# Kernel optimization log

Measured on AMD Instinct MI355X. Metric: run time of the kernel, lower is better.

The kernel has to match this reference:

```python
import jax, jax.numpy as jnp
import numpy as np

T = 1024
V = 512
K_BINS = jnp.array([1, 2, 3, 4, 5, 6, 7, 8, 12, 16, 24, 32, 48, 64, 96, 128], dtype=jnp.int32)
SPLIT_T = T // 2                      # int(T * 0.5)
CW = max(4, T // 20)                  # crossfade width = 51
FADE_START = SPLIT_T - CW // 2        # 487
FADE_END = SPLIT_T + CW // 2          # 537


def _early_weight():
    t = jnp.arange(T, dtype=jnp.float32)
    fade = 1.0 - (t - FADE_START) / (FADE_END - FADE_START)
    ew = jnp.where(t < FADE_START, 1.0, jnp.where(t < FADE_END, fade, 0.0))
    return ew.reshape(1, T, 1)


def setup_inputs() -> dict:
    key = jax.random.key(0)
    k = jax.random.split(key, 5)
    B = 64
    return {
        "x": jax.random.normal(k[0], (B, T, V), dtype=jnp.float32),
        "g_early_real": jax.random.normal(k[1], (V, 16), dtype=jnp.float32) * 0.1,
        "g_early_imag": jax.random.normal(k[2], (V, 16), dtype=jnp.float32) * 0.1,
        "g_late_real": jax.random.normal(k[3], (V, 16), dtype=jnp.float32) * 0.1,
        "g_late_imag": jax.random.normal(k[4], (V, 16), dtype=jnp.float32) * 0.1,
    }


def reference(x, g_early_real, g_early_imag, g_late_real, g_late_imag):
    # x: [B, T, V] real. rfft along time.
    X = jnp.fft.rfft(x, n=T, axis=1)              # [B, F, V] complex, F = T//2+1
    xb = X[:, K_BINS, :]                          # [B, K, V]
    # complex gain (1 + gr + i*gi), broadcast [1, K, V]
    g_e = (g_early_real + 1j * g_early_imag).T[None, :, :]
    g_l = (g_late_real + 1j * g_late_imag).T[None, :, :]
    Y_e = X.at[:, K_BINS, :].set(xb * (1.0 + g_e))
    Y_l = X.at[:, K_BINS, :].set(xb * (1.0 + g_l))
    y_early = jnp.fft.irfft(Y_e, n=T, axis=1)     # [B, T, V]
    y_late = jnp.fft.irfft(Y_l, n=T, axis=1)
    ew = _early_weight()
    return ew * y_early + (1.0 - ew) * y_late
```

## Files before the change

### kernel.cpp

```cpp
#include <hip/hip_runtime.h>
#include <math.h>

#define T_LEN 1024
#define VV 512
#define BB 64
#define NB 16
#define ANG_STEP 0.006135923151542565f
#define FADE_S 487
#define FADE_E 537

typedef float v2f __attribute__((ext_vector_type(2)));

__device__ constexpr int KB[NB] = {1,2,3,4,5,6,7,8,12,16,24,32,48,64,96,128};
__device__ constexpr float SGN[NB] = {-1.f, 1.f, -1.f, 1.f, -1.f, 1.f, -1.f, 1.f,
                                       1.f, 1.f,  1.f, 1.f,  1.f, 1.f,  1.f, 1.f};

__global__ __launch_bounds__(512, 1) void k_fused(const float* __restrict__ x,
                                                  const float* __restrict__ ger,
                                                  const float* __restrict__ gei,
                                                  const float* __restrict__ glr,
                                                  const float* __restrict__ gli,
                                                  float* __restrict__ Hg,
                                                  float* __restrict__ out) {
    const int b    = blockIdx.x;
    const int vc   = blockIdx.y;
    const int tid  = threadIdx.x;
    const int wave = tid >> 6;
    const int lane = tid & 63;

    __shared__ __align__(16) float4 tab4[512][8];
    __shared__ __align__(16) float  scr[4 * 128 * 8];

    for (int i = tid; i < 512 * 8; i += 512) {
        int t = i >> 3, m = i & 7;
        int j0 = 2 * m, j1 = 2 * m + 1;
        int idx0 = (KB[j0] * t) & (T_LEN - 1);
        int idx1 = (KB[j1] * t) & (T_LEN - 1);
        float s0, c0, s1, c1;
        sincosf(ANG_STEP * (float)idx0, &s0, &c0);
        sincosf(ANG_STEP * (float)idx1, &s1, &c1);
        tab4[t][m] = make_float4(c0, s0, c1, s1);
    }
    __syncthreads();

    float ar0[NB], ai0[NB], ar1[NB], ai1[NB];
#pragma unroll
    for (int j = 0; j < NB; ++j) { ar0[j] = ai0[j] = ar1[j] = ai1[j] = 0.f; }

    const int trow = wave * 128;
    const int ttab = trow & 511;
    const float2* xrd = (const float2*)(x + ((size_t)b * T_LEN + trow) * VV + vc * 128) + lane;

#define DFT_T(TT, AV)                                               \
    do {                                                            \
        _Pragma("unroll")                                           \
        for (int m = 0; m < 8; ++m) {                               \
            float4 cs = tab4[ttab + (TT)][m];                       \
            ar0[2*m]   = fmaf((AV).x, cs.x, ar0[2*m]);              \
            ai0[2*m]   = fmaf(-(AV).x, cs.y, ai0[2*m]);             \
            ar1[2*m]   = fmaf((AV).y, cs.x, ar1[2*m]);              \
            ai1[2*m]   = fmaf(-(AV).y, cs.y, ai1[2*m]);             \
            ar0[2*m+1] = fmaf((AV).x, cs.z, ar0[2*m+1]);            \
            ai0[2*m+1] = fmaf(-(AV).x, cs.w, ai0[2*m+1]);           \
            ar1[2*m+1] = fmaf((AV).y, cs.z, ar1[2*m+1]);            \
            ai1[2*m+1] = fmaf(-(AV).y, cs.w, ai1[2*m+1]);           \
        }                                                           \
    } while (0)

    {
        float2 a0 = xrd[(size_t)0 * 256];
        float2 a1 = xrd[(size_t)1 * 256];
        float2 a2 = xrd[(size_t)2 * 256];
        float2 a3 = xrd[(size_t)3 * 256];
        float2 a4 = xrd[(size_t)4 * 256];
        float2 a5 = xrd[(size_t)5 * 256];
        float2 a6 = xrd[(size_t)6 * 256];
        float2 a7 = xrd[(size_t)7 * 256];
#pragma unroll 1
        for (int i = 0; i < 120; i += 8) {
            float2 b0 = xrd[(size_t)(i +  8) * 256];
            float2 b1 = xrd[(size_t)(i +  9) * 256];
            float2 b2 = xrd[(size_t)(i + 10) * 256];
            float2 b3 = xrd[(size_t)(i + 11) * 256];
            float2 b4 = xrd[(size_t)(i + 12) * 256];
            float2 b5 = xrd[(size_t)(i + 13) * 256];
            float2 b6 = xrd[(size_t)(i + 14) * 256];
            float2 b7 = xrd[(size_t)(i + 15) * 256];
            DFT_T(i + 0, a0); DFT_T(i + 1, a1); DFT_T(i + 2, a2); DFT_T(i + 3, a3);
            DFT_T(i + 4, a4); DFT_T(i + 5, a5); DFT_T(i + 6, a6); DFT_T(i + 7, a7);
            a0 = b0; a1 = b1; a2 = b2; a3 = b3;
            a4 = b4; a5 = b5; a6 = b6; a7 = b7;
        }
        DFT_T(120, a0); DFT_T(121, a1); DFT_T(122, a2); DFT_T(123, a3);
        DFT_T(124, a4); DFT_T(125, a5); DFT_T(126, a6); DFT_T(127, a7);
    }
#undef DFT_T

    if (wave >= 4) {
#pragma unroll
        for (int j = 0; j < NB; ++j) {
            ar0[j] *= SGN[j]; ai0[j] *= SGN[j];
            ar1[j] *= SGN[j]; ai1[j] *= SGN[j];
        }
    }
    __syncthreads();

    const int v0 = lane * 2;
    float Xre_lo[2], Xre_hi[2], Xim_lo[2], Xim_hi[2];

#define RED_ROUND(SRC0, SRC1, JOFF, DST)                                   \
    do {                                                                   \
        if (wave < 4) {                                                    \
            _Pragma("unroll")                                              \
            for (int jj = 0; jj < 8; ++jj) {                               \
                scr[((size_t)wave * 128 + v0)     * 8 + jj] = SRC0[(JOFF) + jj]; \
                scr[((size_t)wave * 128 + v0 + 1) * 8 + jj] = SRC1[(JOFF) + jj]; \
            }                                                              \
        }                                                                  \
        __syncthreads();                                                   \
        if (wave >= 4) {                                                   \
            const int w2 = wave - 4;                                       \
            _Pragma("unroll")                                              \
            for (int jj = 0; jj < 8; ++jj) {                               \
                scr[((size_t)w2 * 128 + v0)     * 8 + jj] += SRC0[(JOFF) + jj]; \
                scr[((size_t)w2 * 128 + v0 + 1) * 8 + jj] += SRC1[(JOFF) + jj]; \
            }                                                              \
        }                                                                  \
        __syncthreads();                                                   \
        _Pragma("unroll")                                                  \
        for (int q = 0; q < 2; ++q) {                                      \
            const int c  = tid * 2 + q;                                    \
            const int vq = c >> 3, jq = c & 7;                             \
            DST[q] = scr[((size_t)0 * 128 + vq) * 8 + jq]                  \
                   + scr[((size_t)1 * 128 + vq) * 8 + jq]                  \
                   + scr[((size_t)2 * 128 + vq) * 8 + jq]                  \
                   + scr[((size_t)3 * 128 + vq) * 8 + jq];                 \
        }                                                                  \
        __syncthreads();                                                   \
    } while (0)

    RED_ROUND(ar0, ar1, 0, Xre_lo);
    RED_ROUND(ar0, ar1, 8, Xre_hi);
    RED_ROUND(ai0, ai1, 0, Xim_lo);
    RED_ROUND(ai0, ai1, 8, Xim_hi);
#undef RED_ROUND

    const float scale = 2.0f / (float)T_LEN;
    {
        float* hg = Hg + (size_t)b * 64 * VV;
#pragma unroll
        for (int q = 0; q < 2; ++q) {
            const int c  = tid * 2 + q;
            const int vq = c >> 3;
            const int vg = vc * 128 + vq;
#pragma unroll
            for (int half = 0; half < 2; ++half) {
                const int jq = (c & 7) + half * 8;
                const float Xr = half ? Xre_hi[q] : Xre_lo[q];
                const float Xi = half ? Xim_hi[q] : Xim_lo[q];
                float er = ger[vg * NB + jq], ei = gei[vg * NB + jq];
                float lr = glr[vg * NB + jq], li = gli[vg * NB + jq];
                float here  = (Xr * er - Xi * ei) * scale;
                float heimN = -(Xr * ei + Xi * er) * scale;
                float hlre  = (Xr * lr - Xi * li) * scale;
                float hlimN = -(Xr * li + Xi * lr) * scale;
                hg[(size_t)jq * VV + vg]        = here;
                hg[(size_t)(16 + jq) * VV + vg] = heimN;
                hg[(size_t)(32 + jq) * VV + vg] = hlre;
                hg[(size_t)(48 + jq) * VV + vg] = hlimN;
            }
        }
    }
    __syncthreads();

    float hr0[NB], hi0[NB], hr1[NB], hi1[NB];
    {
        const int qb = (wave < 4) ? 0 : 32;
        const float* hgr = Hg + (size_t)b * 64 * VV + vc * 128;
#pragma unroll
        for (int j = 0; j < NB; ++j) {
            const float sg = (wave >= 4) ? SGN[j] : 1.0f;
            hr0[j] = hgr[(size_t)(qb + j) * VV + v0]          * sg;
            hr1[j] = hgr[(size_t)(qb + j) * VV + v0 + 1]      * sg;
            hi0[j] = hgr[(size_t)(qb + 16 + j) * VV + v0]     * sg;
            hi1[j] = hgr[(size_t)(qb + 16 + j) * VV + v0 + 1] * sg;
        }
    }

    v2f* ow = (v2f*)(out + ((size_t)b * T_LEN + trow) * VV + vc * 128) + lane;

#define APPLY_T(TT, AV)                                                       \
    do {                                                                      \
        float s0 = 0.f, s1 = 0.f;                                             \
        _Pragma("unroll")                                                     \
        for (int m = 0; m < 8; ++m) {                                         \
            float4 cs = tab4[ttab + (TT)][m];                                 \
            s0 = fmaf(hr0[2*m], cs.x, s0);   s0 = fmaf(hi0[2*m], cs.y, s0);   \
            s1 = fmaf(hr1[2*m], cs.x, s1);   s1 = fmaf(hi1[2*m], cs.y, s1);   \
            s0 = fmaf(hr0[2*m+1], cs.z, s0); s0 = fmaf(hi0[2*m+1], cs.w, s0); \
            s1 = fmaf(hr1[2*m+1], cs.z, s1); s1 = fmaf(hi1[2*m+1], cs.w, s1); \
        }                                                                     \
        v2f ov; ov.x = (AV).x + s0; ov.y = (AV).y + s1;                       \
        __builtin_nontemporal_store(ov, &ow[(size_t)(TT) * 256]);             \
    } while (0)

    {
        float2 a0 = xrd[(size_t)0 * 256];
        float2 a1 = xrd[(size_t)1 * 256];
        float2 a2 = xrd[(size_t)2 * 256];
        float2 a3 = xrd[(size_t)3 * 256];
        float2 a4 = xrd[(size_t)4 * 256];
        float2 a5 = xrd[(size_t)5 * 256];
        float2 a6 = xrd[(size_t)6 * 256];
        float2 a7 = xrd[(size_t)7 * 256];
#pragma unroll 1
        for (int i = 0; i < 120; i += 8) {
            float2 b0 = xrd[(size_t)(i +  8) * 256];
            float2 b1 = xrd[(size_t)(i +  9) * 256];
            float2 b2 = xrd[(size_t)(i + 10) * 256];
            float2 b3 = xrd[(size_t)(i + 11) * 256];
            float2 b4 = xrd[(size_t)(i + 12) * 256];
            float2 b5 = xrd[(size_t)(i + 13) * 256];
            float2 b6 = xrd[(size_t)(i + 14) * 256];
            float2 b7 = xrd[(size_t)(i + 15) * 256];
            APPLY_T(i + 0, a0); APPLY_T(i + 1, a1); APPLY_T(i + 2, a2); APPLY_T(i + 3, a3);
            APPLY_T(i + 4, a4); APPLY_T(i + 5, a5); APPLY_T(i + 6, a6); APPLY_T(i + 7, a7);
            a0 = b0; a1 = b1; a2 = b2; a3 = b3;
            a4 = b4; a5 = b5; a6 = b6; a7 = b7;
        }
        APPLY_T(120, a0); APPLY_T(121, a1); APPLY_T(122, a2); APPLY_T(123, a3);
        APPLY_T(124, a4); APPLY_T(125, a5); APPLY_T(126, a6); APPLY_T(127, a7);
    }
#undef APPLY_T
}

__global__ __launch_bounds__(512) void k_fixup(const float* __restrict__ x,
                                               const float* __restrict__ H,
                                               float* __restrict__ out) {
    const int b   = blockIdx.x;
    const int tz  = blockIdx.y;
    const int tid = threadIdx.x;
    const int ts  = tz ? 512 : FADE_S;
    const int te  = tz ? FADE_E : 512;
    const int nt  = te - ts;

    __shared__ float2 tab[32][NB];
    for (int i = tid; i < nt * NB; i += 512) {
        int t = i >> 4, j = i & 15;
        int idx = (KB[j] * (ts + t)) & (T_LEN - 1);
        float ss, cc; sincosf(ANG_STEP * (float)idx, &ss, &cc);
        tab[t][j] = make_float2(cc, ss);
    }

    float er[NB], ei[NB], lr[NB], li[NB];
    const float* hp = H + (size_t)b * 64 * VV + tid;
#pragma unroll
    for (int j = 0; j < NB; ++j) {
        er[j] = hp[(size_t)j        * VV];
        ei[j] = hp[(size_t)(16 + j) * VV];
        lr[j] = hp[(size_t)(32 + j) * VV];
        li[j] = hp[(size_t)(48 + j) * VV];
    }
    __syncthreads();

    const float* xrd = x + ((size_t)b * T_LEN + ts) * VV + tid;
    float*       ow  = out + ((size_t)b * T_LEN + ts) * VV + tid;

    for (int t = 0; t < nt; ++t) {
        float av = xrd[(size_t)t * VV];
        const int tg = ts + t;
        float se = 0.f, sl = 0.f;
#pragma unroll
        for (int j = 0; j < NB; ++j) {
            float2 cs = tab[t][j];
            se = fmaf(er[j], cs.x, se); se = fmaf(ei[j], cs.y, se);
            sl = fmaf(lr[j], cs.x, sl); sl = fmaf(li[j], cs.y, sl);
        }
        float w = 1.0f - (float)(tg - FADE_S) * (1.0f / 50.0f);
        ow[(size_t)t * VV] = av + fmaf(w, se - sl, sl);
    }
}

extern "C" void kernel_launch(void* const* d_in, const int* in_sizes, int n_in,
                              void* d_out, int out_size, void* d_ws, size_t ws_size,
                              hipStream_t stream) {
    (void)in_sizes; (void)n_in; (void)out_size; (void)ws_size;
    const float* x   = (const float*)d_in[0];
    const float* ger = (const float*)d_in[1];
    const float* gei = (const float*)d_in[2];
    const float* glr = (const float*)d_in[3];
    const float* gli = (const float*)d_in[4];
    float* out = (float*)d_out;

    float* Hg = (float*)d_ws;

    k_fused<<<dim3(BB, 4), 512, 0, stream>>>(x, ger, gei, glr, gli, Hg, out);
    k_fixup<<<dim3(BB, 2), 512, 0, stream>>>(x, Hg, out);
}
```

Measured before the change: 112.7 us.

## Replace LDS twiddle table with per-thread recurrence rotation of twiddles

Drops the 64KB shared-memory sincos table and its setup, and instead has each thread generate twiddles on the fly with a complex rotation recurrence seeded by sincosf at its row start. This removes the LDS reads from the DFT and apply loops, and the per-wave sign flips, and relaxes launch_bounds to allow more than one block per CU. In exchange it adds 4 FMA-class ops per bin per time step, which raises ALU work. Accumulated rotation error over 128 steps may also reduce accuracy. The prefetch depth is cut from 8 to 4 rows to save registers.

```diff
diff --git a/kernel.cpp b/kernel.cpp
--- a/kernel.cpp
+++ b/kernel.cpp
@@ -12,59 +12,56 @@
 typedef float v2f __attribute__((ext_vector_type(2)));
 
 __device__ constexpr int KB[NB] = {1,2,3,4,5,6,7,8,12,16,24,32,48,64,96,128};
-__device__ constexpr float SGN[NB] = {-1.f, 1.f, -1.f, 1.f, -1.f, 1.f, -1.f, 1.f,
-                                       1.f, 1.f,  1.f, 1.f,  1.f, 1.f,  1.f, 1.f};
-
-__global__ __launch_bounds__(512, 1) void k_fused(const float* __restrict__ x,
-                                                  const float* __restrict__ ger,
-                                                  const float* __restrict__ gei,
-                                                  const float* __restrict__ glr,
-                                                  const float* __restrict__ gli,
-                                                  float* __restrict__ Hg,
-                                                  float* __restrict__ out) {
+__device__ constexpr float CWT[NB] = {
+    0.9999811753f, 0.9999247018f, 0.9998305818f, 0.9996988187f,
+    0.9995294175f, 0.9993223846f, 0.9990777278f, 0.9987954562f,
+    0.9972904567f, 0.9951847267f, 0.9891765100f, 0.9807852804f,
+    0.9569403357f, 0.9238795325f, 0.8314696123f, 0.7071067812f};
+__device__ constexpr float SWT[NB] = {
+    0.0061358846f, 0.0122715383f, 0.0184067299f, 0.0245412285f,
+    0.0306748032f, 0.0368072229f, 0.0429382569f, 0.0490676743f,
+    0.0735645636f, 0.0980171403f, 0.1467304745f, 0.1950903220f,
+    0.2902846773f, 0.3826834324f, 0.5555702330f, 0.7071067812f};
+
+__global__ __launch_bounds__(512) void k_fused(const float* __restrict__ x,
+                                               const float* __restrict__ ger,
+                                               const float* __restrict__ gei,
+                                               const float* __restrict__ glr,
+                                               const float* __restrict__ gli,
+                                               float* __restrict__ Hg,
+                                               float* __restrict__ out) {
     const int b    = blockIdx.x;
     const int vc   = blockIdx.y;
     const int tid  = threadIdx.x;
     const int wave = tid >> 6;
     const int lane = tid & 63;
 
-    __shared__ __align__(16) float4 tab4[512][8];
-    __shared__ __align__(16) float  scr[4 * 128 * 8];
-
-    for (int i = tid; i < 512 * 8; i += 512) {
-        int t = i >> 3, m = i & 7;
-        int j0 = 2 * m, j1 = 2 * m + 1;
-        int idx0 = (KB[j0] * t) & (T_LEN - 1);
-        int idx1 = (KB[j1] * t) & (T_LEN - 1);
-        float s0, c0, s1, c1;
-        sincosf(ANG_STEP * (float)idx0, &s0, &c0);
-        sincosf(ANG_STEP * (float)idx1, &s1, &c1);
-        tab4[t][m] = make_float4(c0, s0, c1, s1);
-    }
-    __syncthreads();
-
-    float ar0[NB], ai0[NB], ar1[NB], ai1[NB];
-#pragma unroll
-    for (int j = 0; j < NB; ++j) { ar0[j] = ai0[j] = ar1[j] = ai1[j] = 0.f; }
+    __shared__ __align__(16) float scr[4 * 128 * 8];
 
     const int trow = wave * 128;
-    const int ttab = trow & 511;
+    const int v0   = lane * 2;
     const float2* xrd = (const float2*)(x + ((size_t)b * T_LEN + trow) * VV + vc * 128) + lane;
 
-#define DFT_T(TT, AV)                                               \
-    do {                                                            \
-        _Pragma("unroll")                                           \
-        for (int m = 0; m < 8; ++m) {                               \
-            float4 cs = tab4[ttab + (TT)][m];                       \
-            ar0[2*m]   = fmaf((AV).x, cs.x, ar0[2*m]);              \
-            ai0[2*m]   = fmaf(-(AV).x, cs.y, ai0[2*m]);             \
-            ar1[2*m]   = fmaf((AV).y, cs.x, ar1[2*m]);              \
-            ai1[2*m]   = fmaf(-(AV).y, cs.y, ai1[2*m]);             \
-            ar0[2*m+1] = fmaf((AV).x, cs.z, ar0[2*m+1]);            \
-            ai0[2*m+1] = fmaf(-(AV).x, cs.w, ai0[2*m+1]);           \
-            ar1[2*m+1] = fmaf((AV).y, cs.z, ar1[2*m+1]);            \
-            ai1[2*m+1] = fmaf(-(AV).y, cs.w, ai1[2*m+1]);           \
-        }                                                           \
+    float ar0[NB], ai0[NB], ar1[NB], ai1[NB], c[NB], s[NB];
+#pragma unroll
+    for (int j = 0; j < NB; ++j) {
+        ar0[j] = ai0[j] = ar1[j] = ai1[j] = 0.f;
+        int n0 = (KB[j] * trow) & (T_LEN - 1);
+        sincosf(ANG_STEP * (float)n0, &s[j], &c[j]);
+    }
+
+#define DFT_STEP(AV)                                            \
+    do {                                                        \
+        _Pragma("unroll")                                       \
+        for (int j = 0; j < NB; ++j) {                          \
+            ar0[j] = fmaf((AV).x, c[j], ar0[j]);                \
+            ai0[j] = fmaf(-(AV).x, s[j], ai0[j]);               \
+            ar1[j] = fmaf((AV).y, c[j], ar1[j]);                \
+            ai1[j] = fmaf(-(AV).y, s[j], ai1[j]);               \
+            float cn = fmaf(c[j], CWT[j], -(s[j] * SWT[j]));    \
+            float sn = fmaf(s[j], CWT[j], c[j] * SWT[j]);       \
+            c[j] = cn; s[j] = sn;                               \
+        }                                                       \
     } while (0)
 
     {
@@ -72,40 +69,19 @@
         float2 a1 = xrd[(size_t)1 * 256];
         float2 a2 = xrd[(size_t)2 * 256];
         float2 a3 = xrd[(size_t)3 * 256];
-        float2 a4 = xrd[(size_t)4 * 256];
-        float2 a5 = xrd[(size_t)5 * 256];
-        float2 a6 = xrd[(size_t)6 * 256];
-        float2 a7 = xrd[(size_t)7 * 256];
 #pragma unroll 1
-        for (int i = 0; i < 120; i += 8) {
-            float2 b0 = xrd[(size_t)(i +  8) * 256];
-            float2 b1 = xrd[(size_t)(i +  9) * 256];
-            float2 b2 = xrd[(size_t)(i + 10) * 256];
-            float2 b3 = xrd[(size_t)(i + 11) * 256];
-            float2 b4 = xrd[(size_t)(i + 12) * 256];
-            float2 b5 = xrd[(size_t)(i + 13) * 256];
-            float2 b6 = xrd[(size_t)(i + 14) * 256];
-            float2 b7 = xrd[(size_t)(i + 15) * 256];
-            DFT_T(i + 0, a0); DFT_T(i + 1, a1); DFT_T(i + 2, a2); DFT_T(i + 3, a3);
-            DFT_T(i + 4, a4); DFT_T(i + 5, a5); DFT_T(i + 6, a6); DFT_T(i + 7, a7);
+        for (int i = 0; i < 124; i += 4) {
+            float2 b0 = xrd[(size_t)(i + 4) * 256];
+            float2 b1 = xrd[(size_t)(i + 5) * 256];
+            float2 b2 = xrd[(size_t)(i + 6) * 256];
+            float2 b3 = xrd[(size_t)(i + 7) * 256];
+            DFT_STEP(a0); DFT_STEP(a1); DFT_STEP(a2); DFT_STEP(a3);
             a0 = b0; a1 = b1; a2 = b2; a3 = b3;
-            a4 = b4; a5 = b5; a6 = b6; a7 = b7;
-        }
-        DFT_T(120, a0); DFT_T(121, a1); DFT_T(122, a2); DFT_T(123, a3);
-        DFT_T(124, a4); DFT_T(125, a5); DFT_T(126, a6); DFT_T(127, a7);
-    }
-#undef DFT_T
-
-    if (wave >= 4) {
-#pragma unroll
-        for (int j = 0; j < NB; ++j) {
-            ar0[j] *= SGN[j]; ai0[j] *= SGN[j];
-            ar1[j] *= SGN[j]; ai1[j] *= SGN[j];
-        }
-    }
-    __syncthreads();
-
-    const int v0 = lane * 2;
+        }
+        DFT_STEP(a0); DFT_STEP(a1); DFT_STEP(a2); DFT_STEP(a3);
+    }
+#undef DFT_STEP
+
     float Xre_lo[2], Xre_hi[2], Xim_lo[2], Xim_hi[2];
 
 #define RED_ROUND(SRC0, SRC1, JOFF, DST)                                   \
@@ -129,8 +105,8 @@
         __syncthreads();                                                   \
         _Pragma("unroll")                                                  \
         for (int q = 0; q < 2; ++q) {                                      \
-            const int c  = tid * 2 + q;                                    \
-            const int vq = c >> 3, jq = c & 7;                             \
+            const int cc = tid * 2 + q;                                    \
+            const int vq = cc >> 3, jq = cc & 7;                           \
             DST[q] = scr[((size_t)0 * 128 + vq) * 8 + jq]                  \
                    + scr[((size_t)1 * 128 + vq) * 8 + jq]                  \
                    + scr[((size_t)2 * 128 + vq) * 8 + jq]                  \
@@ -150,12 +126,12 @@
         float* hg = Hg + (size_t)b * 64 * VV;
 #pragma unroll
         for (int q = 0; q < 2; ++q) {
-            const int c  = tid * 2 + q;
-            const int vq = c >> 3;
+            const int cc = tid * 2 + q;
+            const int vq = cc >> 3;
             const int vg = vc * 128 + vq;
 #pragma unroll
             for (int half = 0; half < 2; ++half) {
-                const int jq = (c & 7) + half * 8;
+                const int jq = (cc & 7) + half * 8;
                 const float Xr = half ? Xre_hi[q] : Xre_lo[q];
                 const float Xi = half ? Xim_hi[q] : Xim_lo[q];
                 float er = ger[vg * NB + jq], ei = gei[vg * NB + jq];
@@ -179,29 +155,35 @@
         const float* hgr = Hg + (size_t)b * 64 * VV + vc * 128;
 #pragma unroll
         for (int j = 0; j < NB; ++j) {
-            const float sg = (wave >= 4) ? SGN[j] : 1.0f;
-            hr0[j] = hgr[(size_t)(qb + j) * VV + v0]          * sg;
-            hr1[j] = hgr[(size_t)(qb + j) * VV + v0 + 1]      * sg;
-            hi0[j] = hgr[(size_t)(qb + 16 + j) * VV + v0]     * sg;
-            hi1[j] = hgr[(size_t)(qb + 16 + j) * VV + v0 + 1] * sg;
+            hr0[j] = hgr[(size_t)(qb + j) * VV + v0];
+            hr1[j] = hgr[(size_t)(qb + j) * VV + v0 + 1];
+            hi0[j] = hgr[(size_t)(qb + 16 + j) * VV + v0];
+            hi1[j] = hgr[(size_t)(qb + 16 + j) * VV + v0 + 1];
+        }
+#pragma unroll
+        for (int j = 0; j < NB; ++j) {
+            int n0 = (KB[j] * trow) & (T_LEN - 1);
+            sincosf(ANG_STEP * (float)n0, &s[j], &c[j]);
         }
     }
 
     v2f* ow = (v2f*)(out + ((size_t)b * T_LEN + trow) * VV + vc * 128) + lane;
 
-#define APPLY_T(TT, AV)                                                       \
-    do {                                                                      \
-        float s0 = 0.f, s1 = 0.f;                                             \
-        _Pragma("unroll")                                                     \
-        for (int m = 0; m < 8; ++m) {                                         \
-            float4 cs = tab4[ttab + (TT)][m];                                 \
-            s0 = fmaf(hr0[2*m], cs.x, s0);   s0 = fmaf(hi0[2*m], cs.y, s0);   \
-            s1 = fmaf(hr1[2*m], cs.x, s1);   s1 = fmaf(hi1[2*m], cs.y, s1);   \
-            s0 = fmaf(hr0[2*m+1], cs.z, s0); s0 = fmaf(hi0[2*m+1], cs.w, s0); \
-            s1 = fmaf(hr1[2*m+1], cs.z, s1); s1 = fmaf(hi1[2*m+1], cs.w, s1); \
-        }                                                                     \
-        v2f ov; ov.x = (AV).x + s0; ov.y = (AV).y + s1;                       \
-        __builtin_nontemporal_store(ov, &ow[(size_t)(TT) * 256]);             \
+#define APPLY_STEP(TT, AV)                                      \
+    do {                                                        \
+        float s0 = 0.f, s1 = 0.f;                               \
+        _Pragma("unroll")                                       \
+        for (int j = 0; j < NB; ++j) {                          \
+            s0 = fmaf(hr0[j], c[j], s0);                        \
+            s0 = fmaf(hi0[j], s[j], s0);                        \
+            s1 = fmaf(hr1[j], c[j], s1);                        \
+            s1 = fmaf(hi1[j], s[j], s1);                        \
+            float cn = fmaf(c[j], CWT[j], -(s[j] * SWT[j]));    \
+            float sn = fmaf(s[j], CWT[j], c[j] * SWT[j]);       \
+            c[j] = cn; s[j] = sn;                               \
+        }                                                       \
+        v2f ov; ov.x = (AV).x + s0; ov.y = (AV).y + s1;         \
+        __builtin_nontemporal_store(ov, &ow[(size_t)(TT) * 256]); \
     } while (0)
 
     {
@@ -209,29 +191,20 @@
         float2 a1 = xrd[(size_t)1 * 256];
         float2 a2 = xrd[(size_t)2 * 256];
         float2 a3 = xrd[(size_t)3 * 256];
-        float2 a4 = xrd[(size_t)4 * 256];
-        float2 a5 = xrd[(size_t)5 * 256];
-        float2 a6 = xrd[(size_t)6 * 256];
-        float2 a7 = xrd[(size_t)7 * 256];
 #pragma unroll 1
-        for (int i = 0; i < 120; i += 8) {
-            float2 b0 = xrd[(size_t)(i +  8) * 256];
-            float2 b1 = xrd[(size_t)(i +  9) * 256];
-            float2 b2 = xrd[(size_t)(i + 10) * 256];
-            float2 b3 = xrd[(size_t)(i + 11) * 256];
-            float2 b4 = xrd[(size_t)(i + 12) * 256];
-            float2 b5 = xrd[(size_t)(i + 13) * 256];
-            float2 b6 = xrd[(size_t)(i + 14) * 256];
-            float2 b7 = xrd[(size_t)(i + 15) * 256];
-            APPLY_T(i + 0, a0); APPLY_T(i + 1, a1); APPLY_T(i + 2, a2); APPLY_T(i + 3, a3);
-            APPLY_T(i + 4, a4); APPLY_T(i + 5, a5); APPLY_T(i + 6, a6); APPLY_T(i + 7, a7);
+        for (int i = 0; i < 124; i += 4) {
+            float2 b0 = xrd[(size_t)(i + 4) * 256];
+            float2 b1 = xrd[(size_t)(i + 5) * 256];
+            float2 b2 = xrd[(size_t)(i + 6) * 256];
+            float2 b3 = xrd[(size_t)(i + 7) * 256];
+            APPLY_STEP(i + 0, a0); APPLY_STEP(i + 1, a1);
+            APPLY_STEP(i + 2, a2); APPLY_STEP(i + 3, a3);
             a0 = b0; a1 = b1; a2 = b2; a3 = b3;
-            a4 = b4; a5 = b5; a6 = b6; a7 = b7;
-        }
-        APPLY_T(120, a0); APPLY_T(121, a1); APPLY_T(122, a2); APPLY_T(123, a3);
-        APPLY_T(124, a4); APPLY_T(125, a5); APPLY_T(126, a6); APPLY_T(127, a7);
-    }
-#undef APPLY_T
+        }
+        APPLY_STEP(124, a0); APPLY_STEP(125, a1);
+        APPLY_STEP(126, a2); APPLY_STEP(127, a3);
+    }
+#undef APPLY_STEP
 }
 
 __global__ __launch_bounds__(512) void k_fixup(const float* __restrict__ x,
```

After: 126.2 us. 1.12x slower.
